# Kernel tuning notes

Hardware: AMD Instinct MI355X
Metric: run time of the kernel (lower is better)

Reference implementation:

```python
import jax, jax.numpy as jnp
import numpy as np

B, T, I, H, L, O = 64, 512, 256, 1024, 2, 512


def setup_inputs() -> dict:
    key = jax.random.key(0)
    ks = jax.random.split(key, 11)
    sc = 1.0 / np.sqrt(H).astype(np.float32)
    r = lambda k, shape: jax.random.normal(k, shape, jnp.float32) * sc
    return {
        "x": jax.random.normal(ks[0], (B, T, I), jnp.float32),
        "Wih0": r(ks[1], (H, I)),
        "Whh0": r(ks[2], (H, H)),
        "bih0": r(ks[3], (H,)),
        "bhh0": r(ks[4], (H,)),
        "Wih1": r(ks[5], (H, H)),
        "Whh1": r(ks[6], (H, H)),
        "bih1": r(ks[7], (H,)),
        "bhh1": r(ks[8], (H,)),
        "Wfc": r(ks[9], (O, H)),
        "bfc": r(ks[10], (O,)),
    }


def _rnn_layer(x, Wih, Whh, bih, bhh):
    # x: [B, T, D] -> hidden sequence [B, T, H]; tanh RNN (PyTorch nn.RNN semantics)
    # Precompute the input projection for all timesteps (one big GEMM),
    # leaving only the recurrent GEMM inside the scan.
    xp = jnp.einsum('btd,hd->bth', x, Wih) + bih + bhh  # [B, T, H]
    h0 = jnp.zeros((x.shape[0], Whh.shape[0]), x.dtype)

    def step(h, xt):  # xt: [B, H]
        h = jnp.tanh(xt + h @ Whh.T)
        return h, h

    _, hs = jax.lax.scan(step, h0, jnp.swapaxes(xp, 0, 1))  # [T, B, H]
    return jnp.swapaxes(hs, 0, 1)  # [B, T, H]


def reference(x, Wih0, Whh0, bih0, bhh0, Wih1, Whh1, bih1, bhh1, Wfc, bfc):
    h1 = _rnn_layer(x, Wih0, Whh0, bih0, bhh0)
    h2 = _rnn_layer(h1, Wih1, Whh1, bih1, bhh1)
    last = h2[:, -1, :]                     # [B, H]
    return last @ Wfc.T + bfc               # [B, O]
```

## Files before the change

### kernel.cpp

```cpp
#include <hip/hip_runtime.h>
#include <cmath>

#define BB 64
#define TT 512
#define II 256
#define HH 1024
#define OO 512
#define LAG 24

typedef short bf8 __attribute__((ext_vector_type(8)));
typedef float f32x4 __attribute__((ext_vector_type(4)));
typedef unsigned long long u64;

#define MFMA(a, b, c) __builtin_amdgcn_mfma_f32_16x16x32_bf16((a), (b), (c), 0, 0, 0)

__device__ __forceinline__ unsigned short f2bf(float f) {
    unsigned u = __float_as_uint(f);
    return (unsigned short)((u + 0x7fffu + ((u >> 16) & 1u)) >> 16);
}
__device__ __forceinline__ float bf2f(unsigned short h) {
    return __uint_as_float((unsigned)h << 16);
}
__device__ __forceinline__ void split8(const float* v, bf8& hi, bf8& lo) {
#pragma unroll
    for (int j = 0; j < 8; ++j) {
        unsigned short h = f2bf(v[j]);
        float r = v[j] - bf2f(h);
        hi[j] = (short)h;
        lo[j] = (short)f2bf(r);
    }
}
__device__ __forceinline__ void ld8(float* v, const float* p) {
    *(float4*)v       = *(const float4*)p;
    *(float4*)(v + 4) = *(const float4*)(p + 4);
}
__device__ __forceinline__ bf8 load_h(const void* p) { return *(const bf8*)p; }
__device__ __forceinline__ void store_h16(void* p, u64 a, u64 b) {
    __hip_atomic_store((u64*)p, a, __ATOMIC_RELAXED, __HIP_MEMORY_SCOPE_AGENT);
    __hip_atomic_store((u64*)((char*)p + 8), b, __ATOMIC_RELAXED, __HIP_MEMORY_SCOPE_AGENT);
}
__device__ __forceinline__ unsigned ld_flag(const void* p) {
    return __hip_atomic_load((const unsigned*)p, __ATOMIC_RELAXED, __HIP_MEMORY_SCOPE_AGENT);
}
__device__ __forceinline__ void st_flag(void* p, unsigned v) {
    __hip_atomic_store((unsigned*)p, v, __ATOMIC_RELAXED, __HIP_MEMORY_SCOPE_AGENT);
}
__device__ __forceinline__ void acquire_fence() {
    __builtin_amdgcn_fence(__ATOMIC_ACQUIRE, "agent");
    asm volatile("" ::: "memory");
}

__global__ __launch_bounds__(512, 1) void rnn_lag2(
    const float* __restrict__ x,
    const float* __restrict__ Wih0, const float* __restrict__ Whh0,
    const float* __restrict__ bih0, const float* __restrict__ bhh0,
    const float* __restrict__ Wih1, const float* __restrict__ Whh1,
    const float* __restrict__ bih1, const float* __restrict__ bhh1,
    const float* __restrict__ Wfc,  const float* __restrict__ bfc,
    float* __restrict__ out, float* __restrict__ ws,
    int sm, int fpm)
{
    __shared__ float shmem[5120];
    char* staging = (char*)(shmem + 4608);

    const int tid  = threadIdx.x;
    const int w    = tid >> 6;
    const int lane = tid & 63;
    const int col  = lane & 15;
    const int kg   = lane >> 4;
    const int bid  = blockIdx.x;
    const int grp   = bid & 3;
    const int layer = (bid >> 2) & 1;
    const int slot  = bid >> 3;
    const int rb    = slot * 32;
    const int b0    = grp * 16;

    char* wsB    = (char*)ws;
    char* fA     = wsB;
    char* fB     = wsB + 2048;
    char* h1base = wsB + 4096;
    char* h2base = h1base + (size_t)(sm + 1) * 4 * 65536;

    bf8 wh[2][8], wl[2][8];
    {
        float v[8];
        if (layer == 0) {
            #pragma unroll
            for (int n = 0; n < 2; ++n) {
                ld8(v, Wih0 + (size_t)(rb + n * 16 + col) * II + (w * 32 + kg * 8));
                split8(v, wh[n][4], wl[n][4]);
                #pragma unroll
                for (int c = 0; c < 4; ++c) {
                    ld8(v, Whh0 + (size_t)(rb + n * 16 + col) * HH + ((w * 4 + c) * 32 + kg * 8));
                    split8(v, wh[n][c], wl[n][c]);
                }
            }
        } else {
            #pragma unroll
            for (int n = 0; n < 2; ++n)
                #pragma unroll
                for (int c = 0; c < 4; ++c) {
                    ld8(v, Wih1 + (size_t)(rb + n * 16 + col) * HH + ((w * 4 + c) * 32 + kg * 8));
                    split8(v, wh[n][c], wl[n][c]);
                    ld8(v, Whh1 + (size_t)(rb + n * 16 + col) * HH + ((w * 4 + c) * 32 + kg * 8));
                    split8(v, wh[n][4 + c], wl[n][4 + c]);
                }
        }
    }

    const int n_  = tid >> 8;
    const int ekk = (tid >> 4) & 15;
    const int eb  = tid & 15;
    const int R   = rb + n_ * 16 + ekk;
    const float bsum = layer ? (bih1[R] + bhh1[R]) : (bih0[R] + bhh0[R]);
    const int kk5 = n_ * 16 + ekk;
    const int stg = (eb + 16 * (kk5 >> 3)) * 32 + (kk5 & 7) * 2;

    acquire_fence();

    float xv[8];
    if (layer == 0)
        ld8(xv, x + (size_t)(b0 + col) * TT * II + (w * 32 + kg * 8));

    for (int t = 0; t < TT; ++t) {
        if ((t & fpm) == 0) acquire_fence();

        f32x4 acc0 = {0.f, 0.f, 0.f, 0.f};
        f32x4 acc1 = {0.f, 0.f, 0.f, 0.f};

        if (layer == 0) {
            bf8 xh, xl;
            split8(xv, xh, xl);
            acc0 = MFMA(xh, wh[0][4], acc0); acc0 = MFMA(xh, wl[0][4], acc0);
            acc0 = MFMA(xl, wh[0][4], acc0);
            acc1 = MFMA(xh, wh[1][4], acc1); acc1 = MFMA(xh, wl[1][4], acc1);
            acc1 = MFMA(xl, wh[1][4], acc1);
        }

        if (w == 0) {
            const char* fp;
            int tgt;
            if (layer == 0) {
                fp  = (lane < 32 ? fA : fB) + (size_t)(grp * 32 + (lane & 31)) * 16;
                tgt = (lane < 32) ? t : (t - LAG);
            } else {
                fp  = (lane < 32 ? fB : fA) + (size_t)(grp * 32 + (lane & 31)) * 16;
                tgt = (lane < 32) ? t : (t + 1);
            }
            for (;;) {
                int f = (int)ld_flag(fp);
                if (__all(f >= tgt)) break;
                __builtin_amdgcn_s_sleep(1);
            }
        }
        __syncthreads();

        if (layer == 0) {
            if (t >= 1) {
                const char* h1r = h1base + (size_t)(((t - 1) & sm) * 4 + grp) * 65536;
                #pragma unroll
                for (int c = 0; c < 4; ++c) {
                    const char* p = h1r + (size_t)(w * 4 + c) * 2048 + lane * 32;
                    bf8 hh = load_h(p), hl = load_h(p + 16);
                    acc0 = MFMA(hh, wh[0][c], acc0); acc0 = MFMA(hh, wl[0][c], acc0);
                    acc0 = MFMA(hl, wh[0][c], acc0);
                    acc1 = MFMA(hh, wh[1][c], acc1); acc1 = MFMA(hh, wl[1][c], acc1);
                    acc1 = MFMA(hl, wh[1][c], acc1);
                }
            }
        } else {
            {
                const char* h1r = h1base + (size_t)((t & sm) * 4 + grp) * 65536;
                #pragma unroll
                for (int c = 0; c < 4; ++c) {
                    const char* p = h1r + (size_t)(w * 4 + c) * 2048 + lane * 32;
                    bf8 hh = load_h(p), hl = load_h(p + 16);
                    acc0 = MFMA(hh, wh[0][c], acc0); acc0 = MFMA(hh, wl[0][c], acc0);
                    acc0 = MFMA(hl, wh[0][c], acc0);
                    acc1 = MFMA(hh, wh[1][c], acc1); acc1 = MFMA(hh, wl[1][c], acc1);
                    acc1 = MFMA(hl, wh[1][c], acc1);
                }
            }
            if (t >= 1) {
                const char* h2r = h2base + (size_t)(((t - 1) & sm) * 4 + grp) * 65536;
                #pragma unroll
                for (int c = 0; c < 4; ++c) {
                    const char* p = h2r + (size_t)(w * 4 + c) * 2048 + lane * 32;
                    bf8 hh = load_h(p), hl = load_h(p + 16);
                    acc0 = MFMA(hh, wh[0][4 + c], acc0); acc0 = MFMA(hh, wl[0][4 + c], acc0);
                    acc0 = MFMA(hl, wh[0][4 + c], acc0);
                    acc1 = MFMA(hh, wh[1][4 + c], acc1); acc1 = MFMA(hh, wl[1][4 + c], acc1);
                    acc1 = MFMA(hl, wh[1][4 + c], acc1);
                }
            }
        }

        #pragma unroll
        for (int r = 0; r < 4; ++r) {
            shmem[(w * 2 + 0) * 288 + (kg * 4 + r) * 18 + col] = acc0[r];
            shmem[(w * 2 + 1) * 288 + (kg * 4 + r) * 18 + col] = acc1[r];
        }
        __syncthreads();

        {
            float s = bsum;
            #pragma unroll
            for (int wv = 0; wv < 8; ++wv)
                s += shmem[(wv * 2 + n_) * 288 + eb * 18 + ekk];
            const float val = tanhf(s);
            const unsigned short hi = f2bf(val);
            const unsigned short lo = f2bf(val - bf2f(hi));
            *(unsigned short*)(staging + stg)      = hi;
            *(unsigned short*)(staging + stg + 16) = lo;
        }
        __syncthreads();

        {
            char* hw = (layer ? h2base : h1base)
                     + (size_t)((t & sm) * 4 + grp) * 65536 + (size_t)slot * 2048;
            if (tid < 128) {
                const char* src = staging + tid * 16;
                store_h16(hw + tid * 16, *(const u64*)src, *(const u64*)(src + 8));
            }
        }
        asm volatile("s_waitcnt vmcnt(0)" ::: "memory");
        __syncthreads();
        if (tid == 0)
            st_flag((layer ? fB : fA) + (size_t)(grp * 32 + slot) * 16, (unsigned)(t + 1));

        if (layer == 0 && t + 1 < TT)
            ld8(xv, x + ((size_t)(b0 + col) * TT + (t + 1)) * II + (w * 32 + kg * 8));
    }

    if (tid < 128) {
        while ((int)ld_flag(fB + (size_t)tid * 16) < TT)
            __builtin_amdgcn_s_sleep(2);
    }
    __syncthreads();
    acquire_fence();

    float* Wlds = shmem + 2560;
    ((float4*)Wlds)[tid] = ((const float4*)(Wfc + (size_t)(2 * bid) * HH))[tid];
    __syncthreads();

    float p0 = 0.f, p1 = 0.f;
    {
        const int gr   = lane >> 4;
        const int bsub = lane & 15;
        const char* hb = h2base + (size_t)(((TT - 1) & sm) * 4 + gr) * 65536;
        #pragma unroll 4
        for (int k8 = w * 16; k8 < w * 16 + 16; ++k8) {
            const char* p = hb + (size_t)(k8 >> 2) * 2048
                          + (size_t)(bsub + ((k8 & 3) << 4)) * 32;
            bf8 hi = load_h(p), lo = load_h(p + 16);
            const int kb = k8 * 8;
            #pragma unroll
            for (int j = 0; j < 8; ++j) {
                float f = bf2f((unsigned short)hi[j]) + bf2f((unsigned short)lo[j]);
                p0 += f * Wlds[kb + j];
                p1 += f * Wlds[1024 + kb + j];
            }
        }
    }
    __syncthreads();
    shmem[(w * 64 + lane) * 2 + 0] = p0;
    shmem[(w * 64 + lane) * 2 + 1] = p1;
    __syncthreads();
    if (w < 2) {
        float s = bfc[2 * bid + w];
        #pragma unroll
        for (int j = 0; j < 8; ++j) s += shmem[(j * 64 + lane) * 2 + w];
        out[(size_t)lane * OO + 2 * bid + w] = s;
    }
}

extern "C" void kernel_launch(void* const* d_in, const int* in_sizes, int n_in,
                              void* d_out, int out_size, void* d_ws, size_t ws_size,
                              hipStream_t stream) {
    const float* x    = (const float*)d_in[0];
    const float* Wih0 = (const float*)d_in[1];
    const float* Whh0 = (const float*)d_in[2];
    const float* bih0 = (const float*)d_in[3];
    const float* bhh0 = (const float*)d_in[4];
    const float* Wih1 = (const float*)d_in[5];
    const float* Whh1 = (const float*)d_in[6];
    const float* bih1 = (const float*)d_in[7];
    const float* bhh1 = (const float*)d_in[8];
    const float* Wfc  = (const float*)d_in[9];
    const float* bfc  = (const float*)d_in[10];
    float* out = (float*)d_out;
    float* ws  = (float*)d_ws;

    int depth = (ws_size >= (size_t)4096 + (size_t)2 * 64 * 4 * 65536) ? 64 : 32;
    int sm  = depth - 1;
    int fpm = depth / 2 - 1;

    hipMemsetAsync(d_ws, 0, 4096, stream);

    void* args[] = { (void*)&x,
                     (void*)&Wih0, (void*)&Whh0, (void*)&bih0, (void*)&bhh0,
                     (void*)&Wih1, (void*)&Whh1, (void*)&bih1, (void*)&bhh1,
                     (void*)&Wfc,  (void*)&bfc,  (void*)&out,  (void*)&ws,
                     (void*)&sm,   (void*)&fpm };
    hipLaunchCooperativeKernel((void*)rnn_lag2, dim3(256), dim3(512),
                               args, 0, stream);
}
```

Before: 2.414 ms.

## Split layer-1 flag waits so h1 GEMM overlaps wait on h2 readiness

Layer-1 blocks now wait on the layer-0 flags first, do the h1 input-projection MFMAs, and only then wait on the layer-1 peer flags before the recurrent h2 MFMAs. The recurrent dependency wait therefore overlaps useful work instead of sitting in front of it. The spin loops also drop s_sleep, and the ring buffer depth can grow to 128 when the workspace allows, which loosens producer/consumer coupling between layers. The cost is an extra __syncthreads per step and more polling traffic from busy-spinning.

```diff
diff --git a/kernel.cpp b/kernel.cpp
--- a/kernel.cpp
+++ b/kernel.cpp
@@ -50,7 +50,7 @@
     asm volatile("" ::: "memory");
 }
 
-__global__ __launch_bounds__(512, 1) void rnn_lag2(
+__global__ __launch_bounds__(512, 1) void rnn_lag3(
     const float* __restrict__ x,
     const float* __restrict__ Wih0, const float* __restrict__ Whh0,
     const float* __restrict__ bih0, const float* __restrict__ bhh0,
@@ -135,27 +135,18 @@
             acc0 = MFMA(xl, wh[0][4], acc0);
             acc1 = MFMA(xh, wh[1][4], acc1); acc1 = MFMA(xh, wl[1][4], acc1);
             acc1 = MFMA(xl, wh[1][4], acc1);
-        }
-
-        if (w == 0) {
-            const char* fp;
-            int tgt;
-            if (layer == 0) {
-                fp  = (lane < 32 ? fA : fB) + (size_t)(grp * 32 + (lane & 31)) * 16;
-                tgt = (lane < 32) ? t : (t - LAG);
-            } else {
-                fp  = (lane < 32 ? fB : fA) + (size_t)(grp * 32 + (lane & 31)) * 16;
-                tgt = (lane < 32) ? t : (t + 1);
-            }
-            for (;;) {
-                int f = (int)ld_flag(fp);
-                if (__all(f >= tgt)) break;
-                __builtin_amdgcn_s_sleep(1);
-            }
-        }
-        __syncthreads();
-
-        if (layer == 0) {
+
+            if (w == 0) {
+                const char* fp = (lane < 32 ? fA : fB)
+                               + (size_t)(grp * 32 + (lane & 31)) * 16;
+                const int tgt = (lane < 32) ? t : (t - LAG);
+                for (;;) {
+                    int f = (int)ld_flag(fp);
+                    if (__all(f >= tgt)) break;
+                }
+            }
+            __syncthreads();
+
             if (t >= 1) {
                 const char* h1r = h1base + (size_t)(((t - 1) & sm) * 4 + grp) * 65536;
                 #pragma unroll
@@ -169,6 +160,15 @@
                 }
             }
         } else {
+            if (w == 0) {
+                const char* fp = fA + (size_t)(grp * 32 + (lane & 31)) * 16;
+                const int tgt = t + 1;
+                for (;;) {
+                    int f = (lane < 32) ? (int)ld_flag(fp) : tgt;
+                    if (__all(f >= tgt)) break;
+                }
+            }
+            __syncthreads();
             {
                 const char* h1r = h1base + (size_t)((t & sm) * 4 + grp) * 65536;
                 #pragma unroll
@@ -182,6 +182,15 @@
                 }
             }
             if (t >= 1) {
+                if (w == 0) {
+                    const char* fp = fB + (size_t)(grp * 32 + (lane & 31)) * 16;
+                    const int tgt = t;
+                    for (;;) {
+                        int f = (lane < 32) ? (int)ld_flag(fp) : tgt;
+                        if (__all(f >= tgt)) break;
+                    }
+                }
+                __syncthreads();
                 const char* h2r = h2base + (size_t)(((t - 1) & sm) * 4 + grp) * 65536;
                 #pragma unroll
                 for (int c = 0; c < 4; ++c) {
@@ -291,7 +300,9 @@
     float* out = (float*)d_out;
     float* ws  = (float*)d_ws;
 
-    int depth = (ws_size >= (size_t)4096 + (size_t)2 * 64 * 4 * 65536) ? 64 : 32;
+    int depth = 32;
+    if (ws_size >= (size_t)4096 + (size_t)2 * 128 * 4 * 65536)      depth = 128;
+    else if (ws_size >= (size_t)4096 + (size_t)2 * 64 * 4 * 65536)  depth = 64;
     int sm  = depth - 1;
     int fpm = depth / 2 - 1;
 
@@ -302,6 +313,6 @@
                      (void*)&Wih1, (void*)&Whh1, (void*)&bih1, (void*)&bhh1,
                      (void*)&Wfc,  (void*)&bfc,  (void*)&out,  (void*)&ws,
                      (void*)&sm,   (void*)&fpm };
-    hipLaunchCooperativeKernel((void*)rnn_lag2, dim3(256), dim3(512),
+    hipLaunchCooperativeKernel((void*)rnn_lag3, dim3(256), dim3(512),
                                args, 0, stream);
 }
```

Result: faster. 2.291 ms (-5.1%).
